# Performance work log

Hardware: AMD Instinct MI355X
Metric: run time of the kernel (lower is better)

## Reference

```python
import jax, jax.numpy as jnp
import numpy as np

RES = (512, 512)
MAX_VAL = 100.0
OBJ_WIDTH = 5
N_ITERS = 5
SIGMA = 0.2


def setup_inputs() -> dict:
    key = jax.random.key(0)
    ks = jax.random.split(key, 6)
    H, W = RES
    x = jax.random.uniform(ks[0], (1, H, W, 2), jnp.float32) * 2.0 - 1.0  # query grid in [-1,1]
    boundary_types = jax.random.randint(ks[1], (H, W), 0, 2, jnp.int32)
    boundary_conditions = jax.random.uniform(ks[2], (H, W), jnp.float32)
    B_enc = SIGMA * jax.random.normal(ks[3], (64, 2), jnp.float32)  # GaussianEncoding(0.2, 2, 64)
    Wh = jax.random.normal(ks[4], (4, 128, 128), jnp.float32) / jnp.sqrt(128.0)
    W_out = jax.random.normal(ks[5], (128, 1), jnp.float32) / jnp.sqrt(128.0)
    return {"x": x, "boundary_types": boundary_types,
            "boundary_conditions": boundary_conditions,
            "B_enc": B_enc, "Wh": Wh, "W_out": W_out}


def _box_filter(a, width):
    # width x width mean filter, 'same' padding (F.conv2d with ones/width^2 kernel)
    k = jnp.ones((1, 1, width, width), a.dtype) / float(width * width)
    return jax.lax.conv_general_dilated(a[None, None], k, (1, 1), "SAME")[0, 0]


def _grid_sample_2d(img, grid):
    # img [H,W]; grid [N,2] with (x,y) in [-1,1]; bilinear, align_corners=True, border padding
    H, W = img.shape
    ix = jnp.clip((grid[:, 0] + 1.0) * 0.5 * (W - 1), 0.0, W - 1.0)
    iy = jnp.clip((grid[:, 1] + 1.0) * 0.5 * (H - 1), 0.0, H - 1.0)
    x0 = jnp.floor(ix).astype(jnp.int32)
    y0 = jnp.floor(iy).astype(jnp.int32)
    x1 = jnp.clip(x0 + 1, 0, W - 1)
    y1 = jnp.clip(y0 + 1, 0, H - 1)
    wx = ix - x0
    wy = iy - y0
    return (img[y0, x0] * (1 - wx) * (1 - wy) + img[y0, x1] * wx * (1 - wy)
            + img[y1, x0] * (1 - wx) * wy + img[y1, x1] * wx * wy)


def _solve(V0, C, boundary_types, boundary_conditions):
    # 5 Jacobi-style 8-neighbor stencil passes: free cells take the neighbor
    # average plus local cost; boundary cells are pinned to their conditions.
    free = boundary_types == 0

    def step(V, _):
        Vp = jnp.pad(V, 1, mode="edge")
        nb = (Vp[:-2, :-2] + Vp[:-2, 1:-1] + Vp[:-2, 2:]
              + Vp[1:-1, :-2] + Vp[1:-1, 2:]
              + Vp[2:, :-2] + Vp[2:, 1:-1] + Vp[2:, 2:]) / 8.0
        return jnp.where(free, nb + C, boundary_conditions), None

    V, _ = jax.lax.scan(step, V0, None, length=N_ITERS)
    return V


def reference(x, boundary_types, boundary_conditions, B_enc, Wh, W_out):
    H, W = RES
    free = boundary_types == 0
    # V init: max_val everywhere, boundary cells pinned (obj_inds = boundary_types > 0)
    V0 = jnp.where(free, jnp.float32(MAX_VAL), boundary_conditions)

    # Gaussian random Fourier feature encoding of 0.5 + 0.5*x -> 128 dims
    xq = 0.5 + 0.5 * x.reshape(-1, 2)
    vp = (2.0 * jnp.pi) * (xq @ B_enc.T)            # [N, 64]
    enc = jnp.concatenate([jnp.cos(vp), jnp.sin(vp)], axis=-1)  # [N, 128]

    # FullyFusedMLP: 4 hidden ReLU layers of 128 neurons, linear 1-dim output, no bias
    h = enc
    for i in range(Wh.shape[0]):
        h = jax.nn.relu(h @ Wh[i])
    C = (h @ W_out).reshape(H, W)
    C_pos = jax.nn.relu(C)

    # extra cost: box-filtered obstacle boundary values splashed onto free cells
    obj = boundary_conditions * (boundary_types == 1) * (boundary_conditions > 0)
    extra = _box_filter(obj, OBJ_WIDTH) * free
    Cs = C_pos + extra

    out_grid = _solve(V0, Cs, boundary_types, boundary_conditions)
    out = _grid_sample_2d(out_grid, x.reshape(-1, 2)).reshape(H, W)
    return out, C
```

## Files before the change

### kernel.cpp

```cpp
#include <hip/hip_runtime.h>
#include <hip/hip_bf16.h>


typedef unsigned short ushort_t;
typedef short short8 __attribute__((ext_vector_type(8)));
typedef float floatx16 __attribute__((ext_vector_type(16)));
typedef unsigned int uintx4 __attribute__((ext_vector_type(4)));

#define HH 512
#define WW 512
#define NPIX (HH*WW)

__device__ inline unsigned int pk_bf16(float a, float b) {
    __hip_bfloat162 h = __float22bfloat162_rn(float2{a, b});
    return *(unsigned int*)&h;
}
__device__ inline void async_copy16(void* lds, const void* g) {
    __builtin_amdgcn_global_load_lds(
        (const __attribute__((address_space(1))) unsigned int*)g,
        (__attribute__((address_space(3))) unsigned int*)lds, 16, 0, 0);
}

__global__ __launch_bounds__(256) void prep_kernel(const float* __restrict__ Wh,
                                                   ushort_t* __restrict__ WT) {
    __shared__ float trans[32][129];
    const int t = threadIdx.x;
    const int l = blockIdx.x >> 2, n0 = (blockIdx.x & 3) * 32;
    const int nl = t & 31, k0 = t >> 5;
    #pragma unroll
    for (int pass = 0; pass < 16; ++pass) {
        int k = pass * 8 + k0;
        trans[nl][k] = Wh[l * 16384 + k * 128 + n0 + nl];
    }
    __syncthreads();
    #pragma unroll
    for (int c = 0; c < 2; ++c) {
        int idx = c * 256 + t;
        int nl2 = idx >> 4, P = idx & 15;
        int n = n0 + nl2;
        int cc = P ^ (n & 15);
        int kk = cc * 8;
        unsigned int w0 = pk_bf16(trans[nl2][kk + 0], trans[nl2][kk + 1]);
        unsigned int w1 = pk_bf16(trans[nl2][kk + 2], trans[nl2][kk + 3]);
        unsigned int w2 = pk_bf16(trans[nl2][kk + 4], trans[nl2][kk + 5]);
        unsigned int w3 = pk_bf16(trans[nl2][kk + 6], trans[nl2][kk + 7]);
        ((uint4*)WT)[(l * 128 + n) * 16 + P] = uint4{w0, w1, w2, w3};
    }
}

__global__ __launch_bounds__(512, 2) void mlp_kernel(const float* __restrict__ x,
                                                     const ushort_t* __restrict__ WT,
                                                     const float* __restrict__ benc,
                                                     const float* __restrict__ wout,
                                                     float* __restrict__ C_ws,
                                                     float* __restrict__ outbuf) {
    __shared__ __align__(16) ushort_t wlds[4 * 128 * 128];
    const int tid = threadIdx.x;
    const int lane = tid & 63, wave = tid >> 6;
    const int m = lane & 31, Hh = lane >> 5;

    #pragma unroll
    for (int c2 = 0; c2 < 16; ++c2) {
        int base = c2 * 512 + wave * 64;
        async_copy16(&wlds[base * 8], (const char*)WT + (base + lane) * 16);
    }
    __syncthreads();

    #pragma unroll 1
    for (int t = 0; t < 2; ++t) {
        const int pA = ((t * 256 + blockIdx.x) * 16 + wave * 2 + 0) * 32;
        const int pB = ((t * 256 + blockIdx.x) * 16 + wave * 2 + 1) * 32;

        uintx4 fragA[8], fragB[8];

        {
            float2 xa = ((const float2*)x)[pA + m];
            float2 xb = ((const float2*)x)[pB + m];
            float a0 = 0.5f + 0.5f * xa.x, a1 = 0.5f + 0.5f * xa.y;
            float b0 = 0.5f + 0.5f * xb.x, b1 = 0.5f + 0.5f * xb.y;
            #pragma unroll
            for (int ks = 0; ks < 4; ++ks) {
                #pragma unroll
                for (int jp = 0; jp < 4; ++jp) {
                    int f = ks * 16 + Hh * 8 + jp * 2;
                    float4 bv = *(const float4*)&benc[2 * f];
                    float ta0 = __builtin_amdgcn_fractf(a0 * bv.x + a1 * bv.y);
                    float ta1 = __builtin_amdgcn_fractf(a0 * bv.z + a1 * bv.w);
                    float tb0 = __builtin_amdgcn_fractf(b0 * bv.x + b1 * bv.y);
                    float tb1 = __builtin_amdgcn_fractf(b0 * bv.z + b1 * bv.w);
                    fragA[ks][jp]     = pk_bf16(__builtin_amdgcn_cosf(ta0),
                                                __builtin_amdgcn_cosf(ta1));
                    fragA[ks + 4][jp] = pk_bf16(__builtin_amdgcn_sinf(ta0),
                                                __builtin_amdgcn_sinf(ta1));
                    fragB[ks][jp]     = pk_bf16(__builtin_amdgcn_cosf(tb0),
                                                __builtin_amdgcn_cosf(tb1));
                    fragB[ks + 4][jp] = pk_bf16(__builtin_amdgcn_sinf(tb0),
                                                __builtin_amdgcn_sinf(tb1));
                }
            }
        }

        floatx16 accA[4], accB[4];
        #pragma unroll 1
        for (int l = 0; l < 4; ++l) {
            const ushort_t* wl = wlds + l * 16384;
            #pragma unroll
            for (int i = 0; i < 4; ++i) { accA[i] = (floatx16)(0.0f); accB[i] = (floatx16)(0.0f); }

            #pragma unroll
            for (int ks = 0; ks < 8; ++ks) {
                short8 bfA = __builtin_bit_cast(short8, fragA[ks]);
                short8 bfB = __builtin_bit_cast(short8, fragB[ks]);
                #pragma unroll
                for (int i = 0; i < 4; ++i) {
                    int n = i * 32 + m;
                    int cc = 2 * ks + Hh;
                    short8 av = *(const short8*)&wl[(n << 7) + ((cc ^ (n & 15)) << 3)];
                    accA[i] = __builtin_amdgcn_mfma_f32_32x32x16_bf16(av, bfA, accA[i], 0, 0, 0);
                    accB[i] = __builtin_amdgcn_mfma_f32_32x32x16_bf16(av, bfB, accB[i], 0, 0, 0);
                }
            }

            if (l < 3) {
                #pragma unroll
                for (int ks = 0; ks < 8; ++ks) {
                    const int i = ks >> 1, par = ks & 1;
                    {
                        unsigned int u0 = pk_bf16(fmaxf(accA[i][8 * par + 0], 0.0f),
                                                  fmaxf(accA[i][8 * par + 1], 0.0f));
                        unsigned int u1 = pk_bf16(fmaxf(accA[i][8 * par + 2], 0.0f),
                                                  fmaxf(accA[i][8 * par + 3], 0.0f));
                        unsigned int u2 = pk_bf16(fmaxf(accA[i][8 * par + 4], 0.0f),
                                                  fmaxf(accA[i][8 * par + 5], 0.0f));
                        unsigned int u3 = pk_bf16(fmaxf(accA[i][8 * par + 6], 0.0f),
                                                  fmaxf(accA[i][8 * par + 7], 0.0f));
                        unsigned int s0 = Hh ? u0 : u2, s1 = Hh ? u1 : u3;
                        unsigned int k0 = Hh ? u2 : u0, k1 = Hh ? u3 : u1;
                        unsigned int r0 = (unsigned int)__shfl_xor((int)s0, 32);
                        unsigned int r1 = (unsigned int)__shfl_xor((int)s1, 32);
                        fragA[ks][0] = Hh ? r0 : k0;
                        fragA[ks][1] = Hh ? r1 : k1;
                        fragA[ks][2] = Hh ? k0 : r0;
                        fragA[ks][3] = Hh ? k1 : r1;
                    }
                    {
                        unsigned int u0 = pk_bf16(fmaxf(accB[i][8 * par + 0], 0.0f),
                                                  fmaxf(accB[i][8 * par + 1], 0.0f));
                        unsigned int u1 = pk_bf16(fmaxf(accB[i][8 * par + 2], 0.0f),
                                                  fmaxf(accB[i][8 * par + 3], 0.0f));
                        unsigned int u2 = pk_bf16(fmaxf(accB[i][8 * par + 4], 0.0f),
                                                  fmaxf(accB[i][8 * par + 5], 0.0f));
                        unsigned int u3 = pk_bf16(fmaxf(accB[i][8 * par + 6], 0.0f),
                                                  fmaxf(accB[i][8 * par + 7], 0.0f));
                        unsigned int s0 = Hh ? u0 : u2, s1 = Hh ? u1 : u3;
                        unsigned int k0 = Hh ? u2 : u0, k1 = Hh ? u3 : u1;
                        unsigned int r0 = (unsigned int)__shfl_xor((int)s0, 32);
                        unsigned int r1 = (unsigned int)__shfl_xor((int)s1, 32);
                        fragB[ks][0] = Hh ? r0 : k0;
                        fragB[ks][1] = Hh ? r1 : k1;
                        fragB[ks][2] = Hh ? k0 : r0;
                        fragB[ks][3] = Hh ? k1 : r1;
                    }
                }
            }
        }

        float sA = 0.0f, sB = 0.0f;
        #pragma unroll
        for (int i = 0; i < 4; ++i) {
            #pragma unroll
            for (int rq = 0; rq < 4; ++rq) {
                float4 wv = *(const float4*)&wout[i * 32 + rq * 8 + 4 * Hh];
                sA += fmaxf(accA[i][rq * 4 + 0], 0.0f) * wv.x
                    + fmaxf(accA[i][rq * 4 + 1], 0.0f) * wv.y
                    + fmaxf(accA[i][rq * 4 + 2], 0.0f) * wv.z
                    + fmaxf(accA[i][rq * 4 + 3], 0.0f) * wv.w;
                sB += fmaxf(accB[i][rq * 4 + 0], 0.0f) * wv.x
                    + fmaxf(accB[i][rq * 4 + 1], 0.0f) * wv.y
                    + fmaxf(accB[i][rq * 4 + 2], 0.0f) * wv.z
                    + fmaxf(accB[i][rq * 4 + 3], 0.0f) * wv.w;
            }
        }
        sA += __shfl_xor(sA, 32);
        sB += __shfl_xor(sB, 32);
        if (Hh == 0) {
            C_ws[pA + m] = sA;
            outbuf[NPIX + pA + m] = sA;
            C_ws[pB + m] = sB;
            outbuf[NPIX + pB + m] = sB;
        }
    }
}

__global__ __launch_bounds__(256) void fused_solve_kernel(const int* __restrict__ bt,
                                                          const float* __restrict__ bc,
                                                          const float* __restrict__ C_ws,
                                                          float* __restrict__ Vfin) {
    __shared__ float Va[30 * 32];
    __shared__ float Vb[30 * 32];
    __shared__ float Wp[30 * 32];
    const int tid = threadIdx.x;
    const int gx0 = (blockIdx.x & 31) * 16 - 7, gy0 = (blockIdx.x >> 5) * 16 - 7;

    for (int c = tid; c < 30 * 32; c += 256) {
        int li = c >> 5, lj = c & 31;
        int gi = gy0 + li, gj = gx0 + lj;
        float v = 0.0f;
        if (lj < 30 && gi >= 0 && gi < HH && gj >= 0 && gj < WW) {
            int g = gi * WW + gj;
            float b = bc[g];
            if (bt[g] == 1 && b > 0.0f) v = b;
        }
        Va[c] = v;
    }
    __syncthreads();

    for (int c = tid; c < 30 * 32; c += 256) {
        int li = c >> 5, lj = c & 31;
        int gi = gy0 + li, gj = gx0 + lj;
        float w = -1.0f, v0 = 0.0f;
        if (li >= 2 && li < 28 && lj >= 2 && lj < 28 &&
            gi >= 0 && gi < HH && gj >= 0 && gj < WW) {
            int g = gi * WW + gj;
            if (bt[g] == 0) {
                float s = 0.0f;
                #pragma unroll
                for (int di = 0; di < 5; ++di)
                    #pragma unroll
                    for (int dj = 0; dj < 5; ++dj)
                        s += Va[(li + di - 2) * 32 + lj + dj - 2];
                w = fmaxf(C_ws[g], 0.0f) + s * 0.04f;
                v0 = 100.0f;
            } else {
                float b = bc[g];
                w = -b - 1.0f;
                v0 = b;
            }
        }
        Wp[c] = w;
        Vb[c] = v0;
    }
    __syncthreads();

    float* src = Vb;
    float* dst = Va;
    #pragma unroll 1
    for (int t = 0; t < 5; ++t) {
        for (int c = tid; c < 26 * 32; c += 256) {
            int li = 2 + (c >> 5), lj = c & 31;
            if (lj < 2 || lj >= 28) continue;
            float w = Wp[li * 32 + lj];
            float v;
            if (w < 0.0f) {
                v = -w - 1.0f;
            } else {
                int gi = gy0 + li, gj = gx0 + lj;
                int um = (gi > 0)      ? li - 1 : li;
                int dp = (gi < HH - 1) ? li + 1 : li;
                int lm = (gj > 0)      ? lj - 1 : lj;
                int rp = (gj < WW - 1) ? lj + 1 : lj;
                float s = src[um * 32 + lm] + src[um * 32 + lj] + src[um * 32 + rp]
                        + src[li * 32 + lm]                     + src[li * 32 + rp]
                        + src[dp * 32 + lm] + src[dp * 32 + lj] + src[dp * 32 + rp];
                v = s * 0.125f + w;
            }
            dst[li * 32 + lj] = v;
        }
        __syncthreads();
        float* tmp = src; src = dst; dst = tmp;
    }

    {
        int li = 7 + (tid >> 4), lj = 7 + (tid & 15);
        Vfin[(gy0 + li) * WW + gx0 + lj] = src[li * 32 + lj];
    }
}

__global__ void sample_kernel(const float* __restrict__ x,
                              const float* __restrict__ V,
                              float* __restrict__ out) {
    int idx = blockIdx.x * 256 + threadIdx.x;
    float2 g2 = ((const float2*)x)[idx];
    float ix = (g2.x + 1.0f) * 0.5f * 511.0f;
    float iy = (g2.y + 1.0f) * 0.5f * 511.0f;
    ix = fminf(fmaxf(ix, 0.0f), 511.0f);
    iy = fminf(fmaxf(iy, 0.0f), 511.0f);
    int x0 = (int)floorf(ix), y0 = (int)floorf(iy);
    int x1 = min(x0 + 1, 511), y1 = min(y0 + 1, 511);
    float wx = ix - (float)x0, wy = iy - (float)y0;
    float v00 = V[y0 * 512 + x0], v01 = V[y0 * 512 + x1];
    float v10 = V[y1 * 512 + x0], v11 = V[y1 * 512 + x1];
    float v = v00 * (1.0f - wx) * (1.0f - wy) + v01 * wx * (1.0f - wy)
            + v10 * (1.0f - wx) * wy          + v11 * wx * wy;
    out[idx] = v;
}

extern "C" void kernel_launch(void* const* d_in, const int* in_sizes, int n_in,
                              void* d_out, int out_size, void* d_ws, size_t ws_size,
                              hipStream_t stream) {
    const float* x    = (const float*)d_in[0];
    const int*   bt   = (const int*)d_in[1];
    const float* bc   = (const float*)d_in[2];
    const float* benc = (const float*)d_in[3];
    const float* Wh   = (const float*)d_in[4];
    const float* wout = (const float*)d_in[5];

    char* ws = (char*)d_ws;
    ushort_t* WT   = (ushort_t*)(ws + 4096);
    float*    C_ws = (float*)(ws + 262144);
    float*    Vfin = (float*)(ws + 262144 + 3 * (1 << 20));
    float*    outp = (float*)d_out;

    prep_kernel<<<16, 256, 0, stream>>>(Wh, WT);
    mlp_kernel<<<256, 512, 0, stream>>>(x, WT, benc, wout, C_ws, outp);
    fused_solve_kernel<<<1024, 256, 0, stream>>>(bt, bc, C_ws, Vfin);
    sample_kernel<<<1024, 256, 0, stream>>>(x, Vfin, outp);
}
```

Measured before the change: 138.0 us.

## Unroll MLP layers with ping-pong fragments and per-column-tile accumulation

Replaces the runtime layer loop with four unrolled layer calls. Each layer keeps a single pair of accumulators per 32-column output tile, running all K steps for that tile before converting it to the next layer's bf16 fragments in a ping-pong register buffer. The aim is to shrink live accumulator registers from eight floatx16 to two and let conversion of one tile overlap MFMAs of the next. The cost is more input-fragment registers (two sets), a longer dependent MFMA chain per accumulator, and more code size from full unrolling.

New measurement: 318.1 us. 2.31x slower.

```diff
diff --git a/kernel.cpp b/kernel.cpp
--- a/kernel.cpp
+++ b/kernel.cpp
@@ -48,6 +48,44 @@
     }
 }
 
+__device__ inline uintx4 xform(const floatx16& acc, int par, int Hh) {
+    unsigned int u0 = pk_bf16(fmaxf(acc[8 * par + 0], 0.0f), fmaxf(acc[8 * par + 1], 0.0f));
+    unsigned int u1 = pk_bf16(fmaxf(acc[8 * par + 2], 0.0f), fmaxf(acc[8 * par + 3], 0.0f));
+    unsigned int u2 = pk_bf16(fmaxf(acc[8 * par + 4], 0.0f), fmaxf(acc[8 * par + 5], 0.0f));
+    unsigned int u3 = pk_bf16(fmaxf(acc[8 * par + 6], 0.0f), fmaxf(acc[8 * par + 7], 0.0f));
+    unsigned int s0 = Hh ? u0 : u2, s1 = Hh ? u1 : u3;
+    unsigned int k0 = Hh ? u2 : u0, k1 = Hh ? u3 : u1;
+    unsigned int r0 = (unsigned int)__shfl_xor((int)s0, 32);
+    unsigned int r1 = (unsigned int)__shfl_xor((int)s1, 32);
+    uintx4 f;
+    f[0] = Hh ? r0 : k0;
+    f[1] = Hh ? r1 : k1;
+    f[2] = Hh ? k0 : r0;
+    f[3] = Hh ? k1 : r1;
+    return f;
+}
+
+__device__ inline void run_layer(const ushort_t* __restrict__ wl, int m, int Hh,
+                                 const uintx4 (&iA)[8], const uintx4 (&iB)[8],
+                                 uintx4 (&oA)[8], uintx4 (&oB)[8]) {
+    #pragma unroll
+    for (int i = 0; i < 4; ++i) {
+        floatx16 aA = (floatx16)(0.0f), aB = (floatx16)(0.0f);
+        #pragma unroll
+        for (int ks = 0; ks < 8; ++ks) {
+            int n = i * 32 + m;
+            int cc = 2 * ks + Hh;
+            short8 av = *(const short8*)&wl[(n << 7) + ((cc ^ (n & 15)) << 3)];
+            aA = __builtin_amdgcn_mfma_f32_32x32x16_bf16(av, __builtin_bit_cast(short8, iA[ks]), aA, 0, 0, 0);
+            aB = __builtin_amdgcn_mfma_f32_32x32x16_bf16(av, __builtin_bit_cast(short8, iB[ks]), aB, 0, 0, 0);
+        }
+        oA[2 * i]     = xform(aA, 0, Hh);
+        oA[2 * i + 1] = xform(aA, 1, Hh);
+        oB[2 * i]     = xform(aB, 0, Hh);
+        oB[2 * i + 1] = xform(aB, 1, Hh);
+    }
+}
+
 __global__ __launch_bounds__(512, 2) void mlp_kernel(const float* __restrict__ x,
                                                      const ushort_t* __restrict__ WT,
                                                      const float* __restrict__ benc,
@@ -71,7 +109,7 @@
         const int pA = ((t * 256 + blockIdx.x) * 16 + wave * 2 + 0) * 32;
         const int pB = ((t * 256 + blockIdx.x) * 16 + wave * 2 + 1) * 32;
 
-        uintx4 fragA[8], fragB[8];
+        uintx4 fA[8], fB[8], gA[8], gB[8];
 
         {
             float2 xa = ((const float2*)x)[pA + m];
@@ -88,97 +126,44 @@
                     float ta1 = __builtin_amdgcn_fractf(a0 * bv.z + a1 * bv.w);
                     float tb0 = __builtin_amdgcn_fractf(b0 * bv.x + b1 * bv.y);
                     float tb1 = __builtin_amdgcn_fractf(b0 * bv.z + b1 * bv.w);
-                    fragA[ks][jp]     = pk_bf16(__builtin_amdgcn_cosf(ta0),
-                                                __builtin_amdgcn_cosf(ta1));
-                    fragA[ks + 4][jp] = pk_bf16(__builtin_amdgcn_sinf(ta0),
-                                                __builtin_amdgcn_sinf(ta1));
-                    fragB[ks][jp]     = pk_bf16(__builtin_amdgcn_cosf(tb0),
-                                                __builtin_amdgcn_cosf(tb1));
-                    fragB[ks + 4][jp] = pk_bf16(__builtin_amdgcn_sinf(tb0),
-                                                __builtin_amdgcn_sinf(tb1));
+                    fA[ks][jp]     = pk_bf16(__builtin_amdgcn_cosf(ta0), __builtin_amdgcn_cosf(ta1));
+                    fA[ks + 4][jp] = pk_bf16(__builtin_amdgcn_sinf(ta0), __builtin_amdgcn_sinf(ta1));
+                    fB[ks][jp]     = pk_bf16(__builtin_amdgcn_cosf(tb0), __builtin_amdgcn_cosf(tb1));
+                    fB[ks + 4][jp] = pk_bf16(__builtin_amdgcn_sinf(tb0), __builtin_amdgcn_sinf(tb1));
                 }
             }
         }
 
-        floatx16 accA[4], accB[4];
-        #pragma unroll 1
-        for (int l = 0; l < 4; ++l) {
-            const ushort_t* wl = wlds + l * 16384;
+        run_layer(wlds,             m, Hh, fA, fB, gA, gB);
+        run_layer(wlds + 16384,     m, Hh, gA, gB, fA, fB);
+        run_layer(wlds + 2 * 16384, m, Hh, fA, fB, gA, gB);
+
+        float sA = 0.0f, sB = 0.0f;
+        {
+            const ushort_t* wl = wlds + 3 * 16384;
             #pragma unroll
-            for (int i = 0; i < 4; ++i) { accA[i] = (floatx16)(0.0f); accB[i] = (floatx16)(0.0f); }
-
-            #pragma unroll
-            for (int ks = 0; ks < 8; ++ks) {
-                short8 bfA = __builtin_bit_cast(short8, fragA[ks]);
-                short8 bfB = __builtin_bit_cast(short8, fragB[ks]);
+            for (int i = 0; i < 4; ++i) {
+                floatx16 aA = (floatx16)(0.0f), aB = (floatx16)(0.0f);
                 #pragma unroll
-                for (int i = 0; i < 4; ++i) {
+                for (int ks = 0; ks < 8; ++ks) {
                     int n = i * 32 + m;
                     int cc = 2 * ks + Hh;
                     short8 av = *(const short8*)&wl[(n << 7) + ((cc ^ (n & 15)) << 3)];
-                    accA[i] = __builtin_amdgcn_mfma_f32_32x32x16_bf16(av, bfA, accA[i], 0, 0, 0);
-                    accB[i] = __builtin_amdgcn_mfma_f32_32x32x16_bf16(av, bfB, accB[i], 0, 0, 0);
+                    aA = __builtin_amdgcn_mfma_f32_32x32x16_bf16(av, __builtin_bit_cast(short8, gA[ks]), aA, 0, 0, 0);
+                    aB = __builtin_amdgcn_mfma_f32_32x32x16_bf16(av, __builtin_bit_cast(short8, gB[ks]), aB, 0, 0, 0);
                 }
-            }
-
-            if (l < 3) {
                 #pragma unroll
-                for (int ks = 0; ks < 8; ++ks) {
-                    const int i = ks >> 1, par = ks & 1;
-                    {
-                        unsigned int u0 = pk_bf16(fmaxf(accA[i][8 * par + 0], 0.0f),
-                                                  fmaxf(accA[i][8 * par + 1], 0.0f));
-                        unsigned int u1 = pk_bf16(fmaxf(accA[i][8 * par + 2], 0.0f),
-                                                  fmaxf(accA[i][8 * par + 3], 0.0f));
-                        unsigned int u2 = pk_bf16(fmaxf(accA[i][8 * par + 4], 0.0f),
-                                                  fmaxf(accA[i][8 * par + 5], 0.0f));
-                        unsigned int u3 = pk_bf16(fmaxf(accA[i][8 * par + 6], 0.0f),
-                                                  fmaxf(accA[i][8 * par + 7], 0.0f));
-                        unsigned int s0 = Hh ? u0 : u2, s1 = Hh ? u1 : u3;
-                        unsigned int k0 = Hh ? u2 : u0, k1 = Hh ? u3 : u1;
-                        unsigned int r0 = (unsigned int)__shfl_xor((int)s0, 32);
-                        unsigned int r1 = (unsigned int)__shfl_xor((int)s1, 32);
-                        fragA[ks][0] = Hh ? r0 : k0;
-                        fragA[ks][1] = Hh ? r1 : k1;
-                        fragA[ks][2] = Hh ? k0 : r0;
-                        fragA[ks][3] = Hh ? k1 : r1;
-                    }
-                    {
-                        unsigned int u0 = pk_bf16(fmaxf(accB[i][8 * par + 0], 0.0f),
-                                                  fmaxf(accB[i][8 * par + 1], 0.0f));
-                        unsigned int u1 = pk_bf16(fmaxf(accB[i][8 * par + 2], 0.0f),
-                                                  fmaxf(accB[i][8 * par + 3], 0.0f));
-                        unsigned int u2 = pk_bf16(fmaxf(accB[i][8 * par + 4], 0.0f),
-                                                  fmaxf(accB[i][8 * par + 5], 0.0f));
-                        unsigned int u3 = pk_bf16(fmaxf(accB[i][8 * par + 6], 0.0f),
-                                                  fmaxf(accB[i][8 * par + 7], 0.0f));
-                        unsigned int s0 = Hh ? u0 : u2, s1 = Hh ? u1 : u3;
-                        unsigned int k0 = Hh ? u2 : u0, k1 = Hh ? u3 : u1;
-                        unsigned int r0 = (unsigned int)__shfl_xor((int)s0, 32);
-                        unsigned int r1 = (unsigned int)__shfl_xor((int)s1, 32);
-                        fragB[ks][0] = Hh ? r0 : k0;
-                        fragB[ks][1] = Hh ? r1 : k1;
-                        fragB[ks][2] = Hh ? k0 : r0;
-                        fragB[ks][3] = Hh ? k1 : r1;
-                    }
+                for (int rq = 0; rq < 4; ++rq) {
+                    float4 wv = *(const float4*)&wout[i * 32 + rq * 8 + 4 * Hh];
+                    sA += fmaxf(aA[rq * 4 + 0], 0.0f) * wv.x
+                        + fmaxf(aA[rq * 4 + 1], 0.0f) * wv.y
+                        + fmaxf(aA[rq * 4 + 2], 0.0f) * wv.z
+                        + fmaxf(aA[rq * 4 + 3], 0.0f) * wv.w;
+                    sB += fmaxf(aB[rq * 4 + 0], 0.0f) * wv.x
+                        + fmaxf(aB[rq * 4 + 1], 0.0f) * wv.y
+                        + fmaxf(aB[rq * 4 + 2], 0.0f) * wv.z
+                        + fmaxf(aB[rq * 4 + 3], 0.0f) * wv.w;
                 }
-            }
-        }
-
-        float sA = 0.0f, sB = 0.0f;
-        #pragma unroll
-        for (int i = 0; i < 4; ++i) {
-            #pragma unroll
-            for (int rq = 0; rq < 4; ++rq) {
-                float4 wv = *(const float4*)&wout[i * 32 + rq * 8 + 4 * Hh];
-                sA += fmaxf(accA[i][rq * 4 + 0], 0.0f) * wv.x
-                    + fmaxf(accA[i][rq * 4 + 1], 0.0f) * wv.y
-                    + fmaxf(accA[i][rq * 4 + 2], 0.0f) * wv.z
-                    + fmaxf(accA[i][rq * 4 + 3], 0.0f) * wv.w;
-                sB += fmaxf(accB[i][rq * 4 + 0], 0.0f) * wv.x
-                    + fmaxf(accB[i][rq * 4 + 1], 0.0f) * wv.y
-                    + fmaxf(accB[i][rq * 4 + 2], 0.0f) * wv.z
-                    + fmaxf(accB[i][rq * 4 + 3], 0.0f) * wv.w;
             }
         }
         sA += __shfl_xor(sA, 32);
```
